# Kernel optimization log

Hardware: AMD Instinct MI355X
Metric: run time of the kernel (lower is better)

## Reference

```python
import jax, jax.numpy as jnp
import numpy as np

N, E, W_IN, W_OUT, NUM_CLASS, M = 4096, 5, 512, 128, 16, 1024
NUM_LAYERS, ALPHA, THETA = 64, 0.1, 0.5

def leaky_relu(x):
    return jnp.where(x >= 0, x, 0.01 * x)

def setup_inputs() -> dict:
    key = jax.random.key(0)
    ks = jax.random.split(key, 16)
    u = jax.random.uniform(ks[0], (N, N, E), jnp.float32)
    A = jnp.where(u < 0.01, u, 0.0)
    X = jax.random.normal(ks[1], (N, W_IN), jnp.float32)
    target_x = jax.random.randint(ks[2], (M,), 0, N)
    target = jax.random.randint(ks[3], (M,), 0, NUM_CLASS)
    def xav(k, shape):
        fan_in, fan_out = shape[-2], shape[-1]
        lim = (6.0 / (fan_in + fan_out)) ** 0.5
        return jax.random.uniform(k, shape, jnp.float32, -lim, lim)
    H0 = W_IN + E * W_OUT  # DGCN input width
    return dict(
        A=A, X=X, target_x=target_x, target=target,
        weight=xav(ks[4], (W_IN, W_OUT)),
        attw=xav(ks[5], (1, N)),
        attb=jnp.zeros((1, W_OUT), jnp.float32),
        attq=xav(ks[6], (1, W_OUT)),
        Wg=xav(ks[7], (W_IN, W_IN)), bg=jnp.zeros((W_IN,), jnp.float32),
        W0=xav(ks[8], (H0, W_OUT)), b0=jnp.zeros((W_OUT,), jnp.float32),
        Wconvs=xav(ks[9], (NUM_LAYERS, W_OUT, W_OUT)),
        Wd1=xav(ks[10], (W_OUT, W_OUT)), bd1=jnp.zeros((W_OUT,), jnp.float32),
        W1=xav(ks[11], (W_OUT, W_OUT)), b1=jnp.zeros((W_OUT,), jnp.float32),
        W2=xav(ks[12], (W_OUT, NUM_CLASS)), b2=jnp.zeros((NUM_CLASS,), jnp.float32),
    )

def reference(A, X, target_x, target, weight, attw, attb, attq, Wg, bg, W0, b0,
              Wconvs, Wd1, bd1, W1, b1, W2, b2):
    Ae = jnp.transpose(A, (2, 0, 1))              # [E,N,N]
    I = jnp.eye(N, dtype=A.dtype)
    # gcn_conv feature transform is identical for every edge type (dropout p=0)
    Xw = leaky_relu(leaky_relu(X @ Wg + bg) @ weight)   # [N, w_out]
    # norm(H, add=True): transpose, set diagonal to 1, row-normalize by degree
    Ht = Ae.transpose(0, 2, 1) * (1.0 - I) + I          # [E,N,N]
    deg = Ht.sum(-1)
    dinv = jnp.where(deg > 0, 1.0 / deg, 0.0)
    lgcn = jax.nn.relu(jnp.einsum('enm,md->end', dinv[..., None] * Ht, Xw))  # [E,N,w_out]
    # edge-type attention
    tm = jnp.tanh(jnp.einsum('n,end->ed', attw[0], lgcn) + attb)  # [E,w_out]
    watt = (tm * attq[0]).sum(-1)                                  # [E]
    beta = jax.nn.softmax(watt) * E
    Xcat = (beta[:, None, None] * lgcn).transpose(1, 0, 2).reshape(N, E * W_OUT)
    X_ = jnp.concatenate([Xcat, X], axis=1)       # [N, w_in + E*w_out]
    # DGCN: GCNII stack on binary nonzero pattern of mean adjacency, gcn_norm
    B = (jnp.mean(Ae, 0) != 0).astype(A.dtype)
    Bs = jnp.maximum(B, I)                        # add remaining self-loops
    d = Bs.sum(1)
    dis = jnp.where(d > 0, jax.lax.rsqrt(d), 0.0)
    A_hat = dis[:, None] * Bs * dis[None, :]      # D^-1/2 (B+I) D^-1/2
    x0 = jax.nn.relu(X_ @ W0 + b0)                # [N, w_out]
    betas_l = jnp.log(THETA / jnp.arange(1, NUM_LAYERS + 1, dtype=A.dtype) + 1.0)
    def step(x, inp):
        Wl, bl = inp
        h = A_hat @ x
        h = (1.0 - ALPHA) * h + ALPHA * x0        # initial residual
        x = jax.nn.relu((1.0 - bl) * h + bl * (h @ Wl))  # identity mapping
        return x, None
    x, _ = jax.lax.scan(step, x0, (Wconvs, betas_l))
    Z = leaky_relu(x @ Wd1 + bd1)                 # DGCN lins[1] + outer leaky_relu
    Z = leaky_relu(Z @ W1 + b1)                   # linear1
    y = Z[target_x] @ W2 + b2                     # linear2 on labeled nodes [M,C]
    logp = jax.nn.log_softmax(y, axis=-1)
    loss = -jnp.mean(jnp.take_along_axis(logp, target[:, None], axis=1))
    return loss, y
```

## Files before the change

kernel.cpp:

```cpp
#include <hip/hip_runtime.h>
#include <cstdint>
#include <cmath>

#define NN   4096
#define EE   5
#define WIN  512
#define WOUT 128
#define HH0  1152
#define NLAY 64
#define NCLS 16
#define MT   1024
#define GCAP 96
#define BCAP 320
#define ECAP 48
#define KSPLIT 16
#define KCHUNK 256

typedef __attribute__((ext_vector_type(8))) short     bf16x8_t;
typedef __attribute__((ext_vector_type(8))) unsigned short ushort8_t;
typedef __attribute__((ext_vector_type(4))) float     f32x4_t;

__device__ inline unsigned short f2bf(float f) {
  unsigned int u = __float_as_uint(f);
  unsigned int r = (u + 0x7FFFu + ((u >> 16) & 1u)) >> 16;
  return (unsigned short)r;
}

__device__ __forceinline__ void gload16(const unsigned short* g, unsigned short* l) {
  __builtin_amdgcn_global_load_lds(
      (__attribute__((address_space(1))) void*)g,
      (__attribute__((address_space(3))) void*)l, 16, 0, 0);
}

__global__ __launch_bounds__(256) void gemm_kernel(
    const float* __restrict__ A, const float* __restrict__ W,
    const float* __restrict__ bias, float* __restrict__ C,
    int Mdim, int Kdim, int Ndim, int act) {
  __shared__ __align__(16) float sA[16][68];
  __shared__ __align__(16) float sW[16][64];
  int tid = threadIdx.x;
  int tx = tid & 15, ty = tid >> 4;
  int row0 = blockIdx.y * 64, col0 = blockIdx.x * 64;
  float acc[4][4] = {};
  int mA = tid >> 2;
  int kA = (tid & 3) << 2;
  int kW = tid >> 4;
  int nW = (tid & 15) << 2;
  for (int k0 = 0; k0 < Kdim; k0 += 16) {
    float4 av = *(const float4*)(A + (size_t)(row0 + mA) * Kdim + k0 + kA);
    float4 wv = *(const float4*)(W + (size_t)(k0 + kW) * Ndim + col0 + nW);
    sA[kA + 0][mA] = av.x;
    sA[kA + 1][mA] = av.y;
    sA[kA + 2][mA] = av.z;
    sA[kA + 3][mA] = av.w;
    *(float4*)&sW[kW][nW] = wv;
    __syncthreads();
#pragma unroll
    for (int kk = 0; kk < 16; kk++) {
      float4 a = *(const float4*)&sA[kk][ty << 2];
      float4 b = *(const float4*)&sW[kk][tx << 2];
      acc[0][0] += a.x * b.x; acc[0][1] += a.x * b.y; acc[0][2] += a.x * b.z; acc[0][3] += a.x * b.w;
      acc[1][0] += a.y * b.x; acc[1][1] += a.y * b.y; acc[1][2] += a.y * b.z; acc[1][3] += a.y * b.w;
      acc[2][0] += a.z * b.x; acc[2][1] += a.z * b.y; acc[2][2] += a.z * b.z; acc[2][3] += a.z * b.w;
      acc[3][0] += a.w * b.x; acc[3][1] += a.w * b.y; acc[3][2] += a.w * b.z; acc[3][3] += a.w * b.w;
    }
    __syncthreads();
  }
#pragma unroll
  for (int i = 0; i < 4; i++) {
    int r = row0 + (ty << 2) + i;
#pragma unroll
    for (int jc = 0; jc < 4; jc++) {
      int c = col0 + (tx << 2) + jc;
      float o = acc[i][jc];
      if (bias) o += bias[c];
      if (act == 1) o = fmaxf(o, 0.f);
      else if (act == 2) o = (o >= 0.f) ? o : 0.01f * o;
      C[(size_t)r * Ndim + c] = o;
    }
  }
}

__global__ __launch_bounds__(256) void scan_rows_kernel(
    const float* __restrict__ A, int* __restrict__ fcnt, int* __restrict__ fidx,
    float* __restrict__ fval, int* __restrict__ bcnt, int* __restrict__ bidx) {
  __shared__ int   lbuf[1024];
  __shared__ int   lcnt;
  __shared__ int   ecnt[EE];
  __shared__ int   en2[EE][ECAP];
  __shared__ float ev[EE][ECAP];
  __shared__ int   rbase;
  __shared__ int   gbase[EE];
  int tid = threadIdx.x;
  int n1 = blockIdx.x >> 2;
  int qb = (blockIdx.x & 3) << 10;
  if (tid == 0) lcnt = 0;
  if (tid < EE) ecnt[tid] = 0;
  __syncthreads();
  const float4* src = (const float4*)(A + ((size_t)n1 * NN + qb) * EE);
  float buf[20];
  float4* bf4 = (float4*)buf;
#pragma unroll
  for (int c = 0; c < 5; c++) bf4[c] = src[tid * 5 + c];
  int n2base = qb + tid * 4;
#pragma unroll
  for (int u = 0; u < 4; u++) {
    int n2 = n2base + u;
    if (n2 == n1) continue;
    bool any = false;
#pragma unroll
    for (int e = 0; e < EE; e++) {
      float v = buf[u * 5 + e];
      if (v != 0.f) {
        any = true;
        int s = atomicAdd(&ecnt[e], 1);
        if (s < ECAP) { en2[e][s] = n2; ev[e][s] = v; }
      }
    }
    if (any) {
      int s = atomicAdd(&lcnt, 1);
      lbuf[s] = n2;
    }
  }
  __syncthreads();
  if (tid == 0) rbase = atomicAdd(&bcnt[n1], lcnt);
  if (tid < EE) gbase[tid] = atomicAdd(&fcnt[tid * NN + n1], min(ecnt[tid], ECAP));
  __syncthreads();
  int c = lcnt, rb = rbase;
  for (int s = tid; s < c; s += 256)
    if (rb + s < BCAP) bidx[(size_t)n1 * BCAP + rb + s] = lbuf[s];
#pragma unroll
  for (int e = 0; e < EE; e++) {
    int ec = min(ecnt[e], ECAP), gb = gbase[e];
    size_t base = ((size_t)e * NN + n1) * GCAP;
    for (int s = tid; s < ec; s += 256) {
      if (gb + s < GCAP) {
        fidx[base + gb + s] = en2[e][s];
        fval[base + gb + s] = ev[e][s];
      }
    }
  }
}

__global__ __launch_bounds__(64) void transpose_kernel(
    const int* __restrict__ fcnt, const int* __restrict__ fidx, const float* __restrict__ fval,
    int* __restrict__ gcnt, int* __restrict__ gidx, float* __restrict__ gval) {
  int id = blockIdx.x;
  int n1 = id & (NN - 1);
  int e  = id >> 12;
  int c = min(fcnt[id], GCAP);
  for (int s = threadIdx.x; s < c; s += 64) {
    int   n2 = fidx[(size_t)id * GCAP + s];
    float v  = fval[(size_t)id * GCAP + s];
    int t = e * NN + n2;
    int slot = atomicAdd(&gcnt[t], 1);
    if (slot < GCAP) {
      gidx[(size_t)t * GCAP + slot] = n1;
      gval[(size_t)t * GCAP + slot] = v;
    }
  }
}

__global__ void dinv_dis_kernel(const int* __restrict__ gcnt, const float* __restrict__ gval,
                                float* __restrict__ dinv, const int* __restrict__ bcnt,
                                float* __restrict__ dis) {
  int t = blockIdx.x * 256 + threadIdx.x;
  if (t < EE * NN) {
    int cnt = min(gcnt[t], GCAP);
    float s = 1.0f;
    for (int k = 0; k < cnt; k++) s += gval[(size_t)t * GCAP + k];
    dinv[t] = 1.0f / s;
  }
  if (t < NN) dis[t] = rsqrtf(1.0f + (float)min(bcnt[t], BCAP));
}

__global__ __launch_bounds__(256) void build_ahat_kernel(
    const int* __restrict__ bcnt, const int* __restrict__ bidx,
    const float* __restrict__ dis, unsigned short* __restrict__ Ab) {
  __shared__ unsigned int bits[128];
  int i = blockIdx.x, t = threadIdx.x;
  if (t < 128) bits[t] = 0;
  __syncthreads();
  int cnt = min(bcnt[i], BCAP);
  for (int s = t; s < cnt; s += 256) {
    int j = bidx[(size_t)i * BCAP + s];
    atomicOr(&bits[j >> 5], 1u << (j & 31));
  }
  __syncthreads();
  float di = dis[i];
  int c0 = t * 16;
  unsigned short out[16];
#pragma unroll
  for (int u = 0; u < 16; u++) {
    int j = c0 + u;
    bool on = ((bits[j >> 5] >> (j & 31)) & 1u) || (j == i);
    out[u] = on ? f2bf(di * dis[j]) : (unsigned short)0;
  }
  *(ushort8_t*)&Ab[(size_t)i * NN + c0]     = *(ushort8_t*)&out[0];
  *(ushort8_t*)&Ab[(size_t)i * NN + c0 + 8] = *(ushort8_t*)&out[8];
}

__global__ __launch_bounds__(128) void lgcn_kernel(
    const int* __restrict__ gcnt, const int* __restrict__ gidx, const float* __restrict__ gval,
    const float* __restrict__ dinv, const float* __restrict__ Xw, float* __restrict__ lgcn) {
  int i = blockIdx.x, e = blockIdx.y, d = threadIdx.x;
  int t = e * NN + i;
  int cnt = min(gcnt[t], GCAP);
  __shared__ int   sj[GCAP];
  __shared__ float sv[GCAP];
  for (int s = d; s < cnt; s += 128) {
    sj[s] = gidx[(size_t)t * GCAP + s];
    sv[s] = gval[(size_t)t * GCAP + s];
  }
  __syncthreads();
  float acc = Xw[(size_t)i * WOUT + d];
  for (int s = 0; s < cnt; s++) acc += sv[s] * Xw[(size_t)sj[s] * WOUT + d];
  float r = dinv[t] * acc;
  lgcn[(size_t)t * WOUT + d] = fmaxf(r, 0.f);
}

__global__ void att_partial_kernel(const float* __restrict__ lgcn, const float* __restrict__ attw,
                                   float* __restrict__ tm_pre) {
  int e = blockIdx.y, d = threadIdx.x;
  int nbase = blockIdx.x * 128;
  float acc = 0.f;
  for (int k = 0; k < 128; k++) {
    int n = nbase + k;
    acc += attw[n] * lgcn[((size_t)(e * NN + n)) * WOUT + d];
  }
  atomicAdd(&tm_pre[e * WOUT + d], acc);
}

__global__ void att_final_kernel(const float* __restrict__ tm_pre, const float* __restrict__ attb,
                                 const float* __restrict__ attq, float* __restrict__ beta) {
  int lane = threadIdx.x;
  __shared__ float sw[EE];
  for (int e = 0; e < EE; e++) {
    float v = 0.f;
    for (int d = lane; d < WOUT; d += 64) {
      float tmv = tanhf(tm_pre[e * WOUT + d] + attb[d]);
      v += tmv * attq[d];
    }
    for (int off = 32; off; off >>= 1) v += __shfl_down(v, off, 64);
    if (lane == 0) sw[e] = v;
  }
  __syncthreads();
  if (lane == 0) {
    float mx = sw[0];
    for (int e = 1; e < EE; e++) mx = fmaxf(mx, sw[e]);
    float se = 0.f, ex[EE];
    for (int e = 0; e < EE; e++) { ex[e] = expf(sw[e] - mx); se += ex[e]; }
    for (int e = 0; e < EE; e++) beta[e] = ex[e] / se * (float)EE;
  }
}

__global__ void xcat_kernel(const float* __restrict__ lgcn, const float* __restrict__ X,
                            const float* __restrict__ beta, float* __restrict__ Xc) {
  int idx = blockIdx.x * 256 + threadIdx.x;
  const int total = NN * HH0;
  for (; idx < total; idx += gridDim.x * 256) {
    int n = idx / HH0, c = idx - n * HH0;
    float v;
    if (c < EE * WOUT) {
      int e = c >> 7, d = c & 127;
      v = beta[e] * lgcn[((size_t)(e * NN + n)) * WOUT + d];
    } else {
      v = X[(size_t)n * WIN + (c - EE * WOUT)];
    }
    Xc[idx] = v;
  }
}

__global__ __launch_bounds__(256) void xT_convert_kernel(
    const float* __restrict__ x, unsigned short* __restrict__ xT) {
  __shared__ float sh2[128][36];
  int r0 = blockIdx.x * 32, t = threadIdx.x;
  const float4* x4 = (const float4*)(x + (size_t)r0 * WOUT);
#pragma unroll
  for (int q = 0; q < 4; q++) {
    int lin = t + q * 256;
    int r = lin >> 5, c = (lin & 31) * 4;
    float4 v = x4[lin];
    sh2[c + 0][r] = v.x; sh2[c + 1][r] = v.y; sh2[c + 2][r] = v.z; sh2[c + 3][r] = v.w;
  }
  __syncthreads();
  int c = t >> 1, half = t & 1;
  unsigned short tmp[16];
#pragma unroll
  for (int rr = 0; rr < 16; rr++) tmp[rr] = f2bf(sh2[c][half * 16 + rr]);
  *(ushort8_t*)&xT[(size_t)c * NN + r0 + half * 16]     = *(ushort8_t*)&tmp[0];
  *(ushort8_t*)&xT[(size_t)c * NN + r0 + half * 16 + 8] = *(ushort8_t*)&tmp[8];
}

#define SUBSZ (128 * 32)
__global__ __launch_bounds__(256) void spmm_kernel(
    const unsigned short* __restrict__ Ab, const unsigned short* __restrict__ xbT,
    float* __restrict__ P) {
  __shared__ __align__(16) unsigned short sAx[2][2][SUBSZ];
  __shared__ __align__(16) unsigned short sXx[2][2][SUBSZ];
  int t = threadIdx.x;
  int rt = blockIdx.x & 31, kc = blockIdx.x >> 5;
  int r0 = rt * 128, k0 = kc * KCHUNK;
  int wave = t >> 6, lane = t & 63;
  int wr = (wave & 1) * 64, wc = (wave >> 1) * 64;
  int quad = lane >> 4, mrow = lane & 15;
  f32x4_t acc[4][4] = {};

  int srow = wave * 32;
  const unsigned short* gA = Ab  + (size_t)(r0 + srow + (lane >> 2)) * NN + k0 + (lane & 3) * 8;
  const unsigned short* gX = xbT + (size_t)(srow + (lane >> 2)) * NN + k0 + (lane & 3) * 8;

#define STAGE(BUF, KS)                                                          \
  {                                                                             \
    unsigned short* la = &sAx[(BUF)][0][srow * 32];                             \
    unsigned short* lx = &sXx[(BUF)][0][srow * 32];                             \
    _Pragma("unroll")                                                           \
    for (int s = 0; s < 2; s++) {                                               \
      _Pragma("unroll")                                                         \
      for (int h = 0; h < 2; h++) {                                             \
        gload16(gA + (KS) + s * 32 + h * 16 * NN, la + s * SUBSZ + h * 16 * 32);\
        gload16(gX + (KS) + s * 32 + h * 16 * NN, lx + s * SUBSZ + h * 16 * 32);\
      }                                                                         \
    }                                                                           \
  }

  STAGE(0, 0);
  asm volatile("s_waitcnt vmcnt(0)" ::: "memory");
  __builtin_amdgcn_s_barrier();

  int cur = 0;
#pragma unroll
  for (int tt = 0; tt < 4; tt++) {
    if (tt < 3) STAGE(cur ^ 1, (tt + 1) * 64);
    bf16x8_t af[2][4], bfv[2][4];
#pragma unroll
    for (int kk = 0; kk < 2; kk++) {
#pragma unroll
      for (int mi = 0; mi < 4; mi++)
        af[kk][mi] = *(const bf16x8_t*)&sAx[cur][kk][(wr + mi * 16 + mrow) * 32 + quad * 8];
#pragma unroll
      for (int nj = 0; nj < 4; nj++)
        bfv[kk][nj] = *(const bf16x8_t*)&sXx[cur][kk][(wc + nj * 16 + mrow) * 32 + quad * 8];
    }
#pragma unroll
    for (int kk = 0; kk < 2; kk++)
#pragma unroll
      for (int mi = 0; mi < 4; mi++)
#pragma unroll
        for (int nj = 0; nj < 4; nj++)
          acc[mi][nj] = __builtin_amdgcn_mfma_f32_16x16x32_bf16(af[kk][mi], bfv[kk][nj], acc[mi][nj], 0, 0, 0);
    if (tt < 3) {
      asm volatile("s_waitcnt vmcnt(0)" ::: "memory");
      __builtin_amdgcn_s_barrier();
      cur ^= 1;
    }
  }
#undef STAGE

  float* Pk = P + (size_t)kc * (NN * WOUT);
#pragma unroll
  for (int mi = 0; mi < 4; mi++)
#pragma unroll
    for (int nj = 0; nj < 4; nj++) {
#pragma unroll
      for (int r4 = 0; r4 < 4; r4++) {
        int row = r0 + wr + mi * 16 + quad * 4 + r4;
        int col = wc + nj * 16 + mrow;
        Pk[(size_t)row * WOUT + col] = acc[mi][nj][r4];
      }
    }
}

__global__ __launch_bounds__(256) void gcnii_epi_kernel(
    const float* __restrict__ P, const float* __restrict__ x0,
    const float* __restrict__ Wl, float bl,
    float* __restrict__ xout_f32, unsigned short* __restrict__ xoutT, int write_f32) {
  __shared__ float sh2[128][22];
  int r0 = blockIdx.x * 16, t = threadIdx.x;
#pragma unroll
  for (int q = 0; q < 2; q++) {
    int lin = t + q * 256;
    int r = lin >> 5, c = (lin & 31) * 4;
    size_t base4 = ((size_t)(r0 + r) * WOUT + c) >> 2;
    float4 s = {0.f, 0.f, 0.f, 0.f};
#pragma unroll
    for (int kc = 0; kc < KSPLIT; kc++) {
      float4 p = ((const float4*)P)[(size_t)kc * (NN * WOUT / 4) + base4];
      s.x += p.x; s.y += p.y; s.z += p.z; s.w += p.w;
    }
    float4 xv = ((const float4*)x0)[base4];
    s.x = 0.9f * s.x + 0.1f * xv.x;
    s.y = 0.9f * s.y + 0.1f * xv.y;
    s.z = 0.9f * s.z + 0.1f * xv.z;
    s.w = 0.9f * s.w + 0.1f * xv.w;
    sh2[c + 0][r] = s.x; sh2[c + 1][r] = s.y; sh2[c + 2][r] = s.z; sh2[c + 3][r] = s.w;
  }
  __syncthreads();
  int tx = t & 31, ty = t >> 5;
  float2 hv[4];
#pragma unroll
  for (int j = 0; j < 4; j++) hv[j] = *(const float2*)&sh2[tx * 4 + j][ty * 2];
  float o[2][4] = {};
  for (int k = 0; k < WOUT; k++) {
    float2 a = *(const float2*)&sh2[k][ty * 2];
    float4 w = *(const float4*)&Wl[k * WOUT + tx * 4];
    o[0][0] += a.x * w.x; o[0][1] += a.x * w.y; o[0][2] += a.x * w.z; o[0][3] += a.x * w.w;
    o[1][0] += a.y * w.x; o[1][1] += a.y * w.y; o[1][2] += a.y * w.z; o[1][3] += a.y * w.w;
  }
  float c1 = 1.f - bl;
  float y[2][4];
  float hvv[2][4] = {{hv[0].x, hv[1].x, hv[2].x, hv[3].x},
                     {hv[0].y, hv[1].y, hv[2].y, hv[3].y}};
#pragma unroll
  for (int i = 0; i < 2; i++)
#pragma unroll
    for (int j = 0; j < 4; j++)
      y[i][j] = fmaxf(c1 * hvv[i][j] + bl * o[i][j], 0.f);
  if (write_f32) {
#pragma unroll
    for (int i = 0; i < 2; i++) {
      float4 v = {y[i][0], y[i][1], y[i][2], y[i][3]};
      *(float4*)&xout_f32[(size_t)(r0 + ty * 2 + i) * WOUT + tx * 4] = v;
    }
  }
  __syncthreads();
#pragma unroll
  for (int i = 0; i < 2; i++)
#pragma unroll
    for (int j = 0; j < 4; j++)
      sh2[tx * 4 + j][ty * 2 + i] = y[i][j];
  __syncthreads();
  int c = t >> 1, half = t & 1;
  unsigned short tmp[8];
#pragma unroll
  for (int rr = 0; rr < 8; rr++) tmp[rr] = f2bf(sh2[c][half * 8 + rr]);
  *(ushort8_t*)&xoutT[(size_t)c * NN + r0 + half * 8] = *(ushort8_t*)&tmp[0];
}

__global__ __launch_bounds__(256) void head_kernel(
    const float* __restrict__ Z, const int* __restrict__ txv, const int* __restrict__ tgt,
    const float* __restrict__ W2, const float* __restrict__ b2,
    float* __restrict__ out_y, float* __restrict__ lossp) {
  int tid = threadIdx.x;
  int mr = tid >> 4, c = tid & 15;
  int m = blockIdx.x * 16 + mr;
  const float* zr = Z + (size_t)txv[m] * WOUT;
  float acc = b2[c];
  for (int k = 0; k < WOUT; k++) acc += zr[k] * W2[k * NCLS + c];
  out_y[(size_t)m * NCLS + c] = acc;
  float mx = acc;
  for (int off = 8; off; off >>= 1) mx = fmaxf(mx, __shfl_xor(mx, off, 16));
  float ex = expf(acc - mx);
  float se = ex;
  for (int off = 8; off; off >>= 1) se += __shfl_xor(se, off, 16);
  float lse = mx + logf(se);
  float contrib = (c == tgt[m]) ? (lse - acc) : 0.f;
  __shared__ float red[256];
  red[tid] = contrib;
  __syncthreads();
  for (int stp = 128; stp; stp >>= 1) {
    if (tid < stp) red[tid] += red[tid + stp];
    __syncthreads();
  }
  if (tid == 0) lossp[blockIdx.x] = red[0];
}

__global__ void loss_final_kernel(const float* __restrict__ lossp, float* __restrict__ out_loss) {
  int lane = threadIdx.x;
  float v = (lane < 64) ? lossp[lane] : 0.f;
  for (int off = 32; off; off >>= 1) v += __shfl_down(v, off, 64);
  if (lane == 0) out_loss[0] = v / (float)MT;
}

extern "C" void kernel_launch(void* const* d_in, const int* in_sizes, int n_in,
                              void* d_out, int out_size, void* d_ws, size_t ws_size,
                              hipStream_t stream) {
  const float* A      = (const float*)d_in[0];
  const float* X      = (const float*)d_in[1];
  const int*   txv    = (const int*)d_in[2];
  const int*   tgt    = (const int*)d_in[3];
  const float* weight = (const float*)d_in[4];
  const float* attw   = (const float*)d_in[5];
  const float* attb   = (const float*)d_in[6];
  const float* attq   = (const float*)d_in[7];
  const float* Wg     = (const float*)d_in[8];
  const float* bg     = (const float*)d_in[9];
  const float* W0     = (const float*)d_in[10];
  const float* b0     = (const float*)d_in[11];
  const float* Wconvs = (const float*)d_in[12];
  const float* Wd1    = (const float*)d_in[13];
  const float* bd1    = (const float*)d_in[14];
  const float* W1     = (const float*)d_in[15];
  const float* b1     = (const float*)d_in[16];
  const float* W2     = (const float*)d_in[17];
  const float* b2     = (const float*)d_in[18];

  float* ws  = (float*)d_ws;
  int*   wsi = (int*)d_ws;

  const size_t O_GCNT  = 0;
  const size_t O_BCNT  = 20480;
  const size_t O_FCNT  = 24576;
  const size_t O_DINV  = 45056;
  const size_t O_DIS   = 65536;
  const size_t O_TMPRE = 69632;
  const size_t O_BETA  = 70272;
  const size_t O_LOSSP = 70288;
  const size_t O_GIDX  = 71680;
  const size_t O_GVAL  = O_GIDX + 1966080;
  const size_t O_FIDX  = O_GVAL + 1966080;
  const size_t O_FVAL  = O_FIDX + 1966080;
  const size_t O_BIDX  = O_FVAL + 1966080;
  const size_t O_LGCN  = O_BIDX + 1310720;
  const size_t O_XW    = O_LGCN + 2621440;
  const size_t O_X0    = O_XW   + 524288;
  const size_t O_XA    = O_X0   + 524288;
  const size_t O_XB    = O_XA   + 524288;
  const size_t O_AB    = O_XB   + 524288;
  const size_t O_XBT0  = O_AB   + 8388608;
  const size_t O_XBT1  = O_XBT0 + 262144;
  const size_t O_P     = O_XBT1 + 262144;
  const size_t O_T1    = O_FVAL;
  const size_t O_XCAT  = O_GIDX;

  hipMemsetAsync(ws + O_GCNT, 0, 45056 * 4, stream);
  hipMemsetAsync(ws + O_TMPRE, 0, 640 * 4, stream);

  dim3 blk(256);
  gemm_kernel<<<dim3(WIN / 64, NN / 64), blk, 0, stream>>>(X, Wg, bg, ws + O_T1, NN, WIN, WIN, 2);
  gemm_kernel<<<dim3(WOUT / 64, NN / 64), blk, 0, stream>>>(ws + O_T1, weight, nullptr, ws + O_XW, NN, WIN, WOUT, 2);
  scan_rows_kernel<<<NN * 4, 256, 0, stream>>>(A, wsi + O_FCNT, wsi + O_FIDX, ws + O_FVAL,
                                               wsi + O_BCNT, wsi + O_BIDX);
  transpose_kernel<<<EE * NN, 64, 0, stream>>>(wsi + O_FCNT, wsi + O_FIDX, ws + O_FVAL,
                                               wsi + O_GCNT, wsi + O_GIDX, ws + O_GVAL);
  dinv_dis_kernel<<<80, 256, 0, stream>>>(wsi + O_GCNT, ws + O_GVAL, ws + O_DINV,
                                          wsi + O_BCNT, ws + O_DIS);
  build_ahat_kernel<<<NN, 256, 0, stream>>>(wsi + O_BCNT, wsi + O_BIDX, ws + O_DIS,
                                            (unsigned short*)(ws + O_AB));
  lgcn_kernel<<<dim3(NN, EE), 128, 0, stream>>>(wsi + O_GCNT, wsi + O_GIDX, ws + O_GVAL,
                                                ws + O_DINV, ws + O_XW, ws + O_LGCN);
  att_partial_kernel<<<dim3(32, EE), 128, 0, stream>>>(ws + O_LGCN, attw, ws + O_TMPRE);
  att_final_kernel<<<1, 64, 0, stream>>>(ws + O_TMPRE, attb, attq, ws + O_BETA);
  xcat_kernel<<<4096, 256, 0, stream>>>(ws + O_LGCN, X, ws + O_BETA, ws + O_XCAT);
  gemm_kernel<<<dim3(WOUT / 64, NN / 64), blk, 0, stream>>>(ws + O_XCAT, W0, b0, ws + O_X0, NN, HH0, WOUT, 1);
  xT_convert_kernel<<<NN / 32, 256, 0, stream>>>(ws + O_X0, (unsigned short*)(ws + O_XBT0));
  for (int l = 0; l < NLAY; l++) {
    float bl = logf(0.5f / (float)(l + 1) + 1.0f);
    const unsigned short* xin = (const unsigned short*)(ws + ((l & 1) ? O_XBT1 : O_XBT0));
    unsigned short* xoT = (unsigned short*)(ws + ((l & 1) ? O_XBT0 : O_XBT1));
    spmm_kernel<<<32 * KSPLIT, 256, 0, stream>>>((const unsigned short*)(ws + O_AB), xin, ws + O_P);
    gcnii_epi_kernel<<<NN / 16, 256, 0, stream>>>(ws + O_P, ws + O_X0,
                                                  Wconvs + (size_t)l * WOUT * WOUT, bl,
                                                  ws + O_XA, xoT, (l == NLAY - 1) ? 1 : 0);
  }
  gemm_kernel<<<dim3(WOUT / 64, NN / 64), blk, 0, stream>>>(ws + O_XA, Wd1, bd1, ws + O_XB, NN, WOUT, WOUT, 2);
  gemm_kernel<<<dim3(WOUT / 64, NN / 64), blk, 0, stream>>>(ws + O_XB, W1, b1, ws + O_X0, NN, WOUT, WOUT, 2);
  head_kernel<<<MT / 16, 256, 0, stream>>>(ws + O_X0, txv, tgt, W2, b2,
                                           (float*)d_out + 1, ws + O_LOSSP);
  loss_final_kernel<<<1, 64, 0, stream>>>(ws + O_LOSSP, (float*)d_out);
}
```

Baseline: 2.663 ms.

## Retile dense A_hat GEMM to 64-row tiles with halved K-split

```diff
diff --git a/kernel.cpp b/kernel.cpp
--- a/kernel.cpp
+++ b/kernel.cpp
@@ -13,8 +13,9 @@
 #define GCAP 96
 #define BCAP 320
 #define ECAP 48
-#define KSPLIT 16
-#define KCHUNK 256
+#define KSPLIT 8
+#define KCHUNK 512
+#define NTILE  8
 
 typedef __attribute__((ext_vector_type(8))) short     bf16x8_t;
 typedef __attribute__((ext_vector_type(8))) unsigned short ushort8_t;
@@ -292,36 +293,41 @@
   *(ushort8_t*)&xT[(size_t)c * NN + r0 + half * 16 + 8] = *(ushort8_t*)&tmp[8];
 }
 
-#define SUBSZ (128 * 32)
 __global__ __launch_bounds__(256) void spmm_kernel(
     const unsigned short* __restrict__ Ab, const unsigned short* __restrict__ xbT,
     float* __restrict__ P) {
-  __shared__ __align__(16) unsigned short sAx[2][2][SUBSZ];
-  __shared__ __align__(16) unsigned short sXx[2][2][SUBSZ];
+  __shared__ __align__(16) unsigned short sT[2][12288];
   int t = threadIdx.x;
-  int rt = blockIdx.x & 31, kc = blockIdx.x >> 5;
-  int r0 = rt * 128, k0 = kc * KCHUNK;
+  int rt = blockIdx.x & 63, kc = blockIdx.x >> 6;
+  int r0 = rt * 64, k0 = kc * KCHUNK;
   int wave = t >> 6, lane = t & 63;
-  int wr = (wave & 1) * 64, wc = (wave >> 1) * 64;
+  int wr = (wave & 1) * 32, wc = (wave >> 1) * 64;
   int quad = lane >> 4, mrow = lane & 15;
-  f32x4_t acc[4][4] = {};
-
-  int srow = wave * 32;
-  const unsigned short* gA = Ab  + (size_t)(r0 + srow + (lane >> 2)) * NN + k0 + (lane & 3) * 8;
-  const unsigned short* gX = xbT + (size_t)(srow + (lane >> 2)) * NN + k0 + (lane & 3) * 8;
-
-#define STAGE(BUF, KS)                                                          \
-  {                                                                             \
-    unsigned short* la = &sAx[(BUF)][0][srow * 32];                             \
-    unsigned short* lx = &sXx[(BUF)][0][srow * 32];                             \
-    _Pragma("unroll")                                                           \
-    for (int s = 0; s < 2; s++) {                                               \
-      _Pragma("unroll")                                                         \
-      for (int h = 0; h < 2; h++) {                                             \
-        gload16(gA + (KS) + s * 32 + h * 16 * NN, la + s * SUBSZ + h * 16 * 32);\
-        gload16(gX + (KS) + s * 32 + h * 16 * NN, lx + s * SUBSZ + h * 16 * 32);\
-      }                                                                         \
-    }                                                                           \
+  f32x4_t acc[2][4] = {};
+
+  const unsigned short* gq[6];
+  int lq[6];
+#pragma unroll
+  for (int q = 0; q < 6; q++) {
+    int c = wave * 6 + q;
+    if (c < 8) {
+      int sub = c >> 2, rb = c & 3;
+      gq[q] = Ab + (size_t)(r0 + rb * 16 + (lane >> 2)) * NN + k0 + sub * 32 + (lane & 3) * 8;
+      lq[q] = sub * 2048 + rb * 512;
+    } else {
+      int cc = c - 8;
+      int sub = cc >> 3, rb = cc & 7;
+      gq[q] = xbT + (size_t)(rb * 16 + (lane >> 2)) * NN + k0 + sub * 32 + (lane & 3) * 8;
+      lq[q] = 4096 + sub * 4096 + rb * 512;
+    }
+  }
+
+#define STAGE(BUF, TS)                                         \
+  {                                                            \
+    unsigned short* lb = &sT[(BUF)][0];                        \
+    _Pragma("unroll")                                          \
+    for (int q = 0; q < 6; q++)                                \
+      gload16(gq[q] + (TS) * 64, lb + lq[q]);                  \
   }
 
   STAGE(0, 0);
@@ -329,27 +335,27 @@
   __builtin_amdgcn_s_barrier();
 
   int cur = 0;
-#pragma unroll
-  for (int tt = 0; tt < 4; tt++) {
-    if (tt < 3) STAGE(cur ^ 1, (tt + 1) * 64);
-    bf16x8_t af[2][4], bfv[2][4];
+  for (int tt = 0; tt < NTILE; tt++) {
+    if (tt < NTILE - 1) STAGE(cur ^ 1, tt + 1);
+    const unsigned short* base = &sT[cur][0];
+    bf16x8_t af[2][2], bfv[2][4];
 #pragma unroll
     for (int kk = 0; kk < 2; kk++) {
 #pragma unroll
-      for (int mi = 0; mi < 4; mi++)
-        af[kk][mi] = *(const bf16x8_t*)&sAx[cur][kk][(wr + mi * 16 + mrow) * 32 + quad * 8];
+      for (int mi = 0; mi < 2; mi++)
+        af[kk][mi] = *(const bf16x8_t*)&base[kk * 2048 + (wr + mi * 16 + mrow) * 32 + quad * 8];
 #pragma unroll
       for (int nj = 0; nj < 4; nj++)
-        bfv[kk][nj] = *(const bf16x8_t*)&sXx[cur][kk][(wc + nj * 16 + mrow) * 32 + quad * 8];
+        bfv[kk][nj] = *(const bf16x8_t*)&base[4096 + kk * 4096 + (wc + nj * 16 + mrow) * 32 + quad * 8];
     }
 #pragma unroll
     for (int kk = 0; kk < 2; kk++)
 #pragma unroll
-      for (int mi = 0; mi < 4; mi++)
+      for (int mi = 0; mi < 2; mi++)
 #pragma unroll
         for (int nj = 0; nj < 4; nj++)
           acc[mi][nj] = __builtin_amdgcn_mfma_f32_16x16x32_bf16(af[kk][mi], bfv[kk][nj], acc[mi][nj], 0, 0, 0);
-    if (tt < 3) {
+    if (tt < NTILE - 1) {
       asm volatile("s_waitcnt vmcnt(0)" ::: "memory");
       __builtin_amdgcn_s_barrier();
       cur ^= 1;
@@ -359,7 +365,7 @@
 
   float* Pk = P + (size_t)kc * (NN * WOUT);
 #pragma unroll
-  for (int mi = 0; mi < 4; mi++)
+  for (int mi = 0; mi < 2; mi++)
 #pragma unroll
     for (int nj = 0; nj < 4; nj++) {
 #pragma unroll
@@ -548,7 +554,7 @@
     float bl = logf(0.5f / (float)(l + 1) + 1.0f);
     const unsigned short* xin = (const unsigned short*)(ws + ((l & 1) ? O_XBT1 : O_XBT0));
     unsigned short* xoT = (unsigned short*)(ws + ((l & 1) ? O_XBT0 : O_XBT1));
-    spmm_kernel<<<32 * KSPLIT, 256, 0, stream>>>((const unsigned short*)(ws + O_AB), xin, ws + O_P);
+    spmm_kernel<<<64 * KSPLIT, 256, 0, stream>>>((const unsigned short*)(ws + O_AB), xin, ws + O_P);
     gcnii_epi_kernel<<<NN / 16, 256, 0, stream>>>(ws + O_P, ws + O_X0,
                                                   Wconvs + (size_t)l * WOUT * WOUT, bl,
                                                   ws + O_XA, xoT, (l == NLAY - 1) ? 1 : 0);
```

New measurement: 2.386 ms (median of 2 runs). -10.4%, faster.
